# Performance work log

Hardware: AMD Instinct MI355X
Metric: run time of the kernel (lower is better)

The kernel has to match this reference:

```python
import jax, jax.numpy as jnp
from jax import lax
import numpy as np

B = 2048
N = 10  # wires on q_device0
C64 = jnp.complex64

# fixed gate matrices (qubit ordering matches wire-list order)
S_ = jnp.array([[1, 0], [0, 1j]], C64)
T_ = jnp.array([[1, 0], [0, np.exp(1j * np.pi / 4)]], C64)
SX_ = 0.5 * jnp.array([[1 + 1j, 1 - 1j], [1 - 1j, 1 + 1j]], C64)
Y_ = jnp.array([[0, -1j], [1j, 0]], C64)
CNOT_ = jnp.array([[1, 0, 0, 0], [0, 1, 0, 0], [0, 0, 0, 1], [0, 0, 1, 0]], C64)
CZ_ = jnp.diag(jnp.array([1, 1, 1, -1], C64))
CY_ = jnp.array([[1, 0, 0, 0], [0, 1, 0, 0], [0, 0, 0, -1j], [0, 0, 1j, 0]], C64)
SWAP_ = jnp.array([[1, 0, 0, 0], [0, 0, 1, 0], [0, 1, 0, 0], [0, 0, 0, 1]], C64)
_cs = np.eye(8); _cs[[5, 6]] = _cs[[6, 5]]  # CSWAP: |101> <-> |110>
CSWAP_ = jnp.array(_cs, C64)
_tf = np.eye(8); _tf[[6, 7]] = _tf[[7, 6]]  # Toffoli: |110> <-> |111>
TOFF_ = jnp.array(_tf, C64)

# parametrized single-qubit gate builders; t scalar -> [2,2], t [B] -> [B,2,2]
def _rx(t):
    c = jnp.cos(t / 2).astype(C64)
    s = -1j * jnp.sin(t / 2).astype(C64)
    return jnp.stack([jnp.stack([c, s], -1), jnp.stack([s, c], -1)], -2)

def _ry(t):
    c = jnp.cos(t / 2).astype(C64)
    s = jnp.sin(t / 2).astype(C64)
    return jnp.stack([jnp.stack([c, -s], -1), jnp.stack([s, c], -1)], -2)

def _rz(t):
    a = jnp.exp(-0.5j * t.astype(C64))
    b = jnp.exp(0.5j * t.astype(C64))
    z = jnp.zeros_like(a)
    return jnp.stack([jnp.stack([a, z], -1), jnp.stack([z, b], -1)], -2)

def _phase(t):
    e = jnp.exp(1j * t.astype(C64))
    o = jnp.ones_like(e)
    z = jnp.zeros_like(e)
    return jnp.stack([jnp.stack([o, z], -1), jnp.stack([z, e], -1)], -2)

def _rot(phi, th, om):  # RZ(om) RY(th) RZ(phi), pennylane/torchquantum convention
    c = jnp.cos(th / 2).astype(C64)
    s = jnp.sin(th / 2).astype(C64)
    p = phi.astype(C64); w = om.astype(C64)
    m00 = jnp.exp(-0.5j * (p + w)) * c
    m01 = -jnp.exp(0.5j * (p - w)) * s
    m10 = jnp.exp(-0.5j * (p - w)) * s
    m11 = jnp.exp(0.5j * (p + w)) * c
    return jnp.stack([jnp.stack([m00, m01], -1), jnp.stack([m10, m11], -1)], -2)

def _apply1(psi, U, w):  # psi: [B]+(2,)*N, U: [2,2] or [B,2,2]
    s = jnp.moveaxis(psi, w + 1, 1)
    if U.ndim == 2:
        s = jnp.einsum('ij,bj...->bi...', U, s)
    else:
        s = jnp.einsum('bij,bj...->bi...', U, s)
    return jnp.moveaxis(s, 1, w + 1)

def _applyk(psi, U, wires):  # fixed k-qubit gate, U: [2^k, 2^k]
    k = len(wires)
    axes = tuple(w + 1 for w in wires)
    s = jnp.moveaxis(psi, axes, tuple(range(1, k + 1)))
    sh = s.shape
    s = s.reshape((sh[0], 2 ** k) + sh[k + 1:])
    s = jnp.einsum('ij,bj...->bi...', U, s)
    return jnp.moveaxis(s.reshape(sh), tuple(range(1, k + 1)), axes)

def _forward(x, conv1_w, conv1_b, conv2_w, conv2_b, fc1_w, fc1_b, fc2_w, fc2_b,
             theta0, theta_rz, theta_ps, rot_p):
    dn = ('NCHW', 'OIHW', 'NCHW')
    h = lax.conv_general_dilated(x, conv1_w, (1, 1), 'VALID', dimension_numbers=dn)
    h = jax.nn.relu(h + conv1_b[None, :, None, None])
    h = lax.conv_general_dilated(h, conv2_w, (1, 1), 'VALID', dimension_numbers=dn)
    h = jax.nn.relu(h + conv2_b[None, :, None, None])
    h = lax.reduce_window(h, -jnp.inf, lax.max, (1, 1, 2, 2), (1, 1, 2, 2), 'VALID')
    h = h.reshape(h.shape[0], -1)  # [B, 9216], dropout = identity (eval)
    h = jax.nn.relu(h @ fc1_w.T + fc1_b)
    a = jax.nn.sigmoid(h @ fc2_w.T + fc2_b) * (2.0 * np.pi)  # angles [B, 10]
    bsz = a.shape[0]
    psi = jnp.zeros((bsz, 2 ** N), C64).at[:, 0].set(1.0).reshape((bsz,) + (2,) * N)
    trz = jnp.reshape(theta_rz, ())
    tps = jnp.reshape(theta_ps, ())
    for k in range(N):                      # TrainableRxAll
        psi = _apply1(psi, _rx(theta0[k]), k)
    for k in range(N):                      # RxAll with input angles
        psi = _apply1(psi, _rx(a[:, k]), k)
    psi = _apply1(psi, _rx(a[:, 1]), 1)
    psi = _apply1(psi, _rx(jnp.asarray(-np.pi / 4, jnp.float32)), 5)  # q_layer2 fixed
    psi = _apply1(psi, _ry(a[:, 2]), 2)
    psi = _apply1(psi, _rz(a[:, 3]), 3)
    psi = _apply1(psi, S_, 4)
    psi = _apply1(psi, T_, 5)
    psi = _apply1(psi, _rz(trz), 6)         # q_layer3
    psi = _apply1(psi, SX_, 7)
    # (q_device1 ops on a separate 3-wire device do not affect the output)
    psi = _applyk(psi, CZ_, (0, 5))
    psi = _applyk(psi, CNOT_, (0, 5))
    psi = _applyk(psi, CY_, (0, 5))
    psi = _applyk(psi, CY_, (3, 8))         # q_layer4
    psi = _applyk(psi, SWAP_, (2, 3))
    psi = _applyk(psi, CSWAP_, (4, 5, 6))
    psi = _applyk(psi, TOFF_, (8, 5, 0))    # q_layer5
    psi = _apply1(psi, _phase(tps), 8)      # q_layer6
    psi = _apply1(psi, _phase(a[:, 7]), 7)
    psi = _apply1(psi, _rot(rot_p[0], rot_p[1], rot_p[2]), 4)  # q_layer7
    psi = _apply1(psi, _rot(a[:, 6], a[:, 7], a[:, 8]), 5)
    axes = tuple(range(1, N + 1))
    evs = [jnp.real(jnp.sum(jnp.conj(psi) * _apply1(psi, Y_, k), axis=axes))
           for k in range(N)]
    ev = jnp.stack(evs, -1)                 # [B, 10] <Y_k>
    return jax.nn.log_softmax(ev, axis=1)


def setup_inputs() -> dict:
    key = jax.random.key(0)
    ks = jax.random.split(key, 13)
    return {
        'x': jax.random.normal(ks[0], (B, 1, 28, 28), jnp.float32),
        'conv1_w': jax.random.normal(ks[1], (32, 1, 3, 3), jnp.float32) * 0.2,
        'conv1_b': jnp.zeros((32,), jnp.float32),
        'conv2_w': jax.random.normal(ks[2], (64, 32, 3, 3), jnp.float32) * 0.05,
        'conv2_b': jnp.zeros((64,), jnp.float32),
        'fc1_w': jax.random.normal(ks[3], (128, 9216), jnp.float32) * 0.01,
        'fc1_b': jnp.zeros((128,), jnp.float32),
        'fc2_w': jax.random.normal(ks[4], (10, 128), jnp.float32) * 0.1,
        'fc2_b': jnp.zeros((10,), jnp.float32),
        'theta0': jax.random.normal(ks[5], (10,), jnp.float32),
        'theta_rz': jax.random.normal(ks[6], (1,), jnp.float32),
        'theta_ps': jax.random.normal(ks[7], (1,), jnp.float32),
        'rot_p': jax.random.normal(ks[8], (3,), jnp.float32),
    }


def reference(x, conv1_w, conv1_b, conv2_w, conv2_b, fc1_w, fc1_b, fc2_w, fc2_b,
              theta0, theta_rz, theta_ps, rot_p):
    return _forward(x, conv1_w, conv1_b, conv2_w, conv2_b, fc1_w, fc1_b, fc2_w, fc2_b,
                    theta0, theta_rz, theta_ps, rot_p)
```

## Files before the change

### kernel.cpp

```cpp
#include <hip/hip_runtime.h>
#include <math.h>

typedef short short8 __attribute__((ext_vector_type(8)));
typedef float f32x4 __attribute__((ext_vector_type(4)));
typedef float f32x16 __attribute__((ext_vector_type(16)));

#define GLB_CP(p) ((const __attribute__((address_space(1))) void*)(p))
#define LDS_CP(p) ((__attribute__((address_space(3))) void*)(p))

__device__ __forceinline__ float2 cmul(float2 a, float2 b) {
    return make_float2(a.x * b.x - a.y * b.y, a.x * b.y + a.y * b.x);
}

__device__ __forceinline__ ushort f2bf(float f) {
    uint u = __float_as_uint(f);
    uint r = (u + 0x7FFFu + ((u >> 16) & 1u)) >> 16;
    return (ushort)r;
}

__global__ __launch_bounds__(256) void prep_kernel(
    const float* __restrict__ c2w, const float* __restrict__ f1w,
    ushort* __restrict__ wt2, ushort* __restrict__ wf1)
{
    int i = blockIdx.x * 256 + threadIdx.x;
    if (i < 18432) {
        int icl = i & 7;
        int t = i >> 3;
        int oc = t & 63;
        int t2 = t >> 6;
        int icg = t2 & 3;
        int tap = t2 >> 2;
        int ic = icg * 8 + icl;
        wt2[i] = f2bf(c2w[(oc * 32 + ic) * 9 + tap]);
    } else if (i < 18432 + 1179648) {
        int j = i - 18432;
        wf1[j] = f2bf(f1w[j]);
    }
}

__global__ __launch_bounds__(256) void conv1_kernel(
    const float* __restrict__ x, const float* __restrict__ w1,
    const float* __restrict__ b1, ushort* __restrict__ h1b)
{
    __shared__ float wl[288];
    __shared__ float bl[32];
    int tid = threadIdx.x;
    for (int e = tid; e < 288; e += 256) wl[e] = w1[e];
    if (tid < 32) bl[tid] = b1[tid];
    __syncthreads();
    int e = blockIdx.x * 256 + tid;
    int icg = e & 3;
    int t = e >> 2;
    int pix = t % 676;
    int b = t / 676;
    int y = pix / 26, xc = pix % 26;
    const float* xp = x + b * 784 + y * 28 + xc;
    float in9[9];
#pragma unroll
    for (int ky = 0; ky < 3; ++ky)
#pragma unroll
        for (int kx = 0; kx < 3; ++kx) in9[ky * 3 + kx] = xp[ky * 28 + kx];
    short8 outv;
#pragma unroll
    for (int o = 0; o < 8; ++o) {
        int oc = icg * 8 + o;
        float acc = bl[oc];
#pragma unroll
        for (int k = 0; k < 9; ++k) acc = fmaf(in9[k], wl[oc * 9 + k], acc);
        outv[o] = (short)f2bf(fmaxf(acc, 0.f));
    }
    *(short8*)&h1b[((b * 4 + icg) * 676 + pix) * 8] = outv;
}

#define EPILOG(ACC0, ACC1, RX, RY)                                                         \
    {                                                                                      \
        int pcolb = (RX) * 4 + 2 * hi;                                                     \
        _Pragma("unroll")                                                                  \
        for (int q = 0; q < 2; ++q) {                                                      \
            int prow = (RY) * 2 + q;                                                       \
            int bs = 8 * q;                                                                \
            float m00 = fmaxf(fmaxf(ACC0[bs], ACC0[bs + 1]), fmaxf(ACC0[bs + 4], ACC0[bs + 5])); \
            float m01 = fmaxf(fmaxf(ACC0[bs + 2], ACC0[bs + 3]), fmaxf(ACC0[bs + 6], ACC0[bs + 7])); \
            uint pk0 = (uint)f2bf(fmaxf(m00 + bias0, 0.f)) | ((uint)f2bf(fmaxf(m01 + bias0, 0.f)) << 16); \
            *(uint*)&pout[lo * 144 + prow * 12 + pcolb] = pk0;                             \
            float m10 = fmaxf(fmaxf(ACC1[bs], ACC1[bs + 1]), fmaxf(ACC1[bs + 4], ACC1[bs + 5])); \
            float m11 = fmaxf(fmaxf(ACC1[bs + 2], ACC1[bs + 3]), fmaxf(ACC1[bs + 6], ACC1[bs + 7])); \
            uint pk1 = (uint)f2bf(fmaxf(m10 + bias1, 0.f)) | ((uint)f2bf(fmaxf(m11 + bias1, 0.f)) << 16); \
            *(uint*)&pout[(lo + 32) * 144 + prow * 12 + pcolb] = pk1;                      \
        }                                                                                  \
    }

__global__ __launch_bounds__(384, 2) void conv2_persist(
    const ushort* __restrict__ h1b, const ushort* __restrict__ wt2,
    const float* __restrict__ c2b, ushort* __restrict__ pooled)
{
    __shared__ __attribute__((aligned(16))) ushort wt_lds[18432];
    __shared__ __attribute__((aligned(16))) ushort in_lds[2][22016];
    int cu = blockIdx.x;
    int tid = threadIdx.x;
    int wave = tid >> 6;
    int lane = tid & 63;
    int lo = lane & 31;
    int hi = lane >> 5;

    for (int c = wave; c < 36; c += 6) {
        const ushort* src = wt2 + (size_t)(c * 64 + lane) * 8;
        __builtin_amdgcn_global_load_lds(GLB_CP(src), LDS_CP(wt_lds + c * 512), 16, 0, 0);
    }
    {
        const ushort* base = h1b + (size_t)(cu * 8) * 21632;
        for (int c = wave; c < 43; c += 6) {
            int e = c * 64 + lane;
            if (e > 2703) e = 2703;
            __builtin_amdgcn_global_load_lds(GLB_CP(base + (size_t)e * 8),
                                             LDS_CP(in_lds[0] + c * 512), 16, 0, 0);
        }
    }
    float bias0 = c2b[lo];
    float bias1 = c2b[lo + 32];
    __syncthreads();

    short8 A0r[9][2];
#pragma unroll
    for (int tap = 0; tap < 9; ++tap)
#pragma unroll
        for (int ks = 0; ks < 2; ++ks)
            A0r[tap][ks] = *(const short8*)&wt_lds[((tap * 4 + ks * 2 + hi) * 64 + lo) * 8];

    int pb[3];
#pragma unroll
    for (int i = 0; i < 3; ++i) {
        int r = wave + 6 * i;
        int rx = r % 3, ry = r / 3;
        int xcoord = rx * 8 + (lo & 7);
        int ycoord = ry * 4 + (lo >> 3);
        pb[i] = ycoord * 26 + xcoord;
    }
    int rx0 = wave % 3, ry0 = wave / 3;
    int rx1 = (wave + 6) % 3, ry1 = (wave + 6) / 3;
    int rx2 = (wave + 12) % 3, ry2 = (wave + 12) / 3;

    for (int j = 0; j < 8; ++j) {
        if (j < 7) {
            const ushort* base = h1b + (size_t)(cu * 8 + j + 1) * 21632;
            ushort* dst = in_lds[(j + 1) & 1];
            for (int c = wave; c < 43; c += 6) {
                int e = c * 64 + lane;
                if (e > 2703) e = 2703;
                __builtin_amdgcn_global_load_lds(GLB_CP(base + (size_t)e * 8),
                                                 LDS_CP(dst + c * 512), 16, 0, 0);
            }
        }

        const ushort* ib = in_lds[j & 1];
        f32x16 aA0 = (f32x16)0.f, aA1 = (f32x16)0.f;
        f32x16 aB0 = (f32x16)0.f, aB1 = (f32x16)0.f;
        f32x16 aC0 = (f32x16)0.f, aC1 = (f32x16)0.f;

#pragma unroll
        for (int tap = 0; tap < 9; ++tap) {
            int off = (tap / 3) * 26 + (tap % 3);
#pragma unroll
            for (int ks = 0; ks < 2; ++ks) {
                short8 a0 = A0r[tap][ks];
                short8 a1 = *(const short8*)&wt_lds[((tap * 4 + ks * 2 + hi) * 64 + 32 + lo) * 8];
                const ushort* ip = &ib[((ks * 2 + hi) * 676 + off) * 8];
                short8 b0 = *(const short8*)(ip + pb[0] * 8);
                short8 b1 = *(const short8*)(ip + pb[1] * 8);
                short8 b2 = *(const short8*)(ip + pb[2] * 8);
                aA0 = __builtin_amdgcn_mfma_f32_32x32x16_bf16(b0, a0, aA0, 0, 0, 0);
                aA1 = __builtin_amdgcn_mfma_f32_32x32x16_bf16(b0, a1, aA1, 0, 0, 0);
                aB0 = __builtin_amdgcn_mfma_f32_32x32x16_bf16(b1, a0, aB0, 0, 0, 0);
                aB1 = __builtin_amdgcn_mfma_f32_32x32x16_bf16(b1, a1, aB1, 0, 0, 0);
                aC0 = __builtin_amdgcn_mfma_f32_32x32x16_bf16(b2, a0, aC0, 0, 0, 0);
                aC1 = __builtin_amdgcn_mfma_f32_32x32x16_bf16(b2, a1, aC1, 0, 0, 0);
            }
        }

        ushort* pout = pooled + (size_t)(cu * 8 + j) * 9216;
        EPILOG(aA0, aA1, rx0, ry0)
        EPILOG(aB0, aB1, rx1, ry1)
        EPILOG(aC0, aC1, rx2, ry2)
        __syncthreads();
    }
}

__global__ __launch_bounds__(256) void fc1_mfma(
    const ushort* __restrict__ pooled, const ushort* __restrict__ wf1,
    float* __restrict__ part)
{
    int bx = blockIdx.x, by = blockIdx.y;
    int tid = threadIdx.x;
    int wid = tid >> 6, lane = tid & 63;
    int lo = lane & 15, hi = lane >> 4;
    int m0 = bx * 32;
    int kb = by * 2304;

    f32x4 acc[2][2];
#pragma unroll
    for (int mt = 0; mt < 2; ++mt)
#pragma unroll
        for (int j = 0; j < 2; ++j) acc[mt][j] = (f32x4)0.f;

    const ushort* arow0 = pooled + (size_t)(m0 + lo) * 9216 + kb + hi * 8;
    const ushort* arow1 = arow0 + 16 * 9216;
    const ushort* brow0 = wf1 + (size_t)(wid * 32 + lo) * 9216 + kb + hi * 8;
    const ushort* brow1 = brow0 + 16 * 9216;

    for (int kt = 0; kt < 72; ++kt) {
        short8 a0 = *(const short8*)(arow0 + kt * 32);
        short8 a1 = *(const short8*)(arow1 + kt * 32);
        short8 b0 = *(const short8*)(brow0 + kt * 32);
        short8 b1 = *(const short8*)(brow1 + kt * 32);
        acc[0][0] = __builtin_amdgcn_mfma_f32_16x16x32_bf16(a0, b0, acc[0][0], 0, 0, 0);
        acc[1][0] = __builtin_amdgcn_mfma_f32_16x16x32_bf16(a1, b0, acc[1][0], 0, 0, 0);
        acc[0][1] = __builtin_amdgcn_mfma_f32_16x16x32_bf16(a0, b1, acc[0][1], 0, 0, 0);
        acc[1][1] = __builtin_amdgcn_mfma_f32_16x16x32_bf16(a1, b1, acc[1][1], 0, 0, 0);
    }
    float* pp = part + (size_t)by * 262144;
#pragma unroll
    for (int mt = 0; mt < 2; ++mt)
#pragma unroll
        for (int j = 0; j < 2; ++j)
#pragma unroll
            for (int r = 0; r < 4; ++r)
                pp[(m0 + mt * 16 + hi * 4 + r) * 128 + wid * 32 + j * 16 + lo] = acc[mt][j][r];
}

__global__ __launch_bounds__(256) void fc1_reduce_kernel(
    const float* __restrict__ part, const float* __restrict__ bias,
    float* __restrict__ outp)
{
    int idx = blockIdx.x * 256 + threadIdx.x;
    float s = 0.f;
#pragma unroll
    for (int ks = 0; ks < 4; ++ks) s += part[ks * 262144 + idx];
    outp[idx] = fmaxf(s + bias[idx & 127], 0.f);
}

__global__ __launch_bounds__(256) void fc2_kernel(
    const float* __restrict__ h, const float* __restrict__ w,
    const float* __restrict__ bias, float* __restrict__ ang)
{
    int idx = blockIdx.x * 256 + threadIdx.x;
    if (idx >= 20480) return;
    int b = idx / 10, n = idx % 10;
    const float* hp = h + b * 128;
    const float* wp = w + n * 128;
    float s = bias[n];
    for (int k = 0; k < 128; ++k) s = fmaf(hp[k], wp[k], s);
    ang[idx] = 6.28318530718f / (1.f + expf(-s));
}

__device__ __forceinline__ void apply_rot2(float2* s, int p, float2 m00, float2 m01,
                                           float2 m10, float2 m11, int tid)
{
    for (int q = tid; q < 512; q += 256) {
        int i0 = ((q >> p) << (p + 1)) | (q & ((1 << p) - 1));
        int i1 = i0 | (1 << p);
        float2 aa = s[i0], bb = s[i1];
        s[i0] = make_float2(m00.x * aa.x - m00.y * aa.y + m01.x * bb.x - m01.y * bb.y,
                            m00.x * aa.y + m00.y * aa.x + m01.x * bb.y + m01.y * bb.x);
        s[i1] = make_float2(m10.x * aa.x - m10.y * aa.y + m11.x * bb.x - m11.y * bb.y,
                            m10.x * aa.y + m10.y * aa.x + m11.x * bb.y + m11.y * bb.x);
    }
}

__global__ __launch_bounds__(256) void quantum_kernel(
    const float* __restrict__ ang, const float* __restrict__ theta0,
    const float* __restrict__ theta_rz, const float* __restrict__ theta_ps,
    const float* __restrict__ rot_p, float* __restrict__ out)
{
    __shared__ float2 s[1024];
    __shared__ float red[40];
    __shared__ float P[64];
    int b = blockIdx.x;
    int tid = threadIdx.x;

    if (tid < 13) {
        if (tid < 10) {
            int k = tid;
            float ak = ang[b * 10 + k];
            float th = theta0[k] + ak;
            if (k == 1) th += ak;
            if (k == 5) th -= 0.78539816339745f;
            float c, sn; sincosf(0.5f * th, &sn, &c);
            float2 v0 = make_float2(c, 0.f), v1 = make_float2(0.f, -sn);
            if (k == 0) v1 = make_float2(-sn, 0.f);
            if (k == 2) { float ca, sa; sincosf(0.5f * ak, &sa, &ca);
                float2 n0 = make_float2(ca * v0.x - sa * v1.x, ca * v0.y - sa * v1.y);
                float2 n1 = make_float2(sa * v0.x + ca * v1.x, sa * v0.y + ca * v1.y);
                v0 = n0; v1 = n1; }
            if (k == 3) { float ca, sa; sincosf(0.5f * ak, &sa, &ca);
                v0 = cmul(v0, make_float2(ca, -sa));
                v1 = cmul(v1, make_float2(ca, sa)); }
            if (k == 4) { float2 t = v1; v1 = make_float2(-t.y, t.x); }
            if (k == 5) { const float r = 0.70710678118655f;
                float2 t = v1; v1 = make_float2(r * (t.x - t.y), r * (t.x + t.y)); }
            if (k == 6) { float ca, sa; sincosf(0.5f * theta_rz[0], &sa, &ca);
                v0 = cmul(v0, make_float2(ca, -sa));
                v1 = cmul(v1, make_float2(ca, sa)); }
            if (k == 7) { float2 p = v0, q = v1;
                v0 = make_float2(0.5f * ((p.x - p.y) + (q.x + q.y)),
                                 0.5f * ((p.x + p.y) + (q.y - q.x)));
                v1 = make_float2(0.5f * ((p.x + p.y) + (q.x - q.y)),
                                 0.5f * ((p.y - p.x) + (q.x + q.y)));
                float c2, s2; sincosf(ak, &s2, &c2);
                v1 = cmul(v1, make_float2(c2, s2)); }
            P[k * 4 + 0] = v0.x; P[k * 4 + 1] = v0.y;
            P[k * 4 + 2] = v1.x; P[k * 4 + 3] = v1.y;
        } else if (tid == 10) {
            float c1, s1; sincosf(theta_ps[0], &s1, &c1);
            P[40] = c1; P[41] = s1;
        } else if (tid == 11) {
            float c, sn; sincosf(0.5f * rot_p[1], &sn, &c);
            float A = 0.5f * (rot_p[0] + rot_p[2]), Bv = 0.5f * (rot_p[0] - rot_p[2]);
            float cA, sA; sincosf(A, &sA, &cA);
            float cB, sB; sincosf(Bv, &sB, &cB);
            P[44] = cA * c;  P[45] = -sA * c;
            P[46] = -cB * sn; P[47] = -sB * sn;
            P[48] = cB * sn;  P[49] = -sB * sn;
            P[50] = cA * c;  P[51] = sA * c;
        } else {
            float a6 = ang[b * 10 + 6], a7 = ang[b * 10 + 7], a8 = ang[b * 10 + 8];
            float c, sn; sincosf(0.5f * a7, &sn, &c);
            float A = 0.5f * (a6 + a8), Bv = 0.5f * (a6 - a8);
            float cA, sA; sincosf(A, &sA, &cA);
            float cB, sB; sincosf(Bv, &sB, &cB);
            P[52] = cA * c;  P[53] = -sA * c;
            P[54] = -cB * sn; P[55] = -sB * sn;
            P[56] = cB * sn;  P[57] = -sB * sn;
            P[58] = cA * c;  P[59] = sA * c;
        }
    }
    __syncthreads();

    float2 v[10][2];
#pragma unroll
    for (int k = 0; k < 10; ++k) {
        int slot = (k == 2) ? 3 : (k == 3) ? 2 : k;
        v[k][0] = make_float2(P[slot * 4], P[slot * 4 + 1]);
        v[k][1] = make_float2(P[slot * 4 + 2], P[slot * 4 + 3]);
    }

    for (int i = tid; i < 1024; i += 256) {
        float2 c = ((i >> 9) & 1) ? v[0][1] : v[0][0];
#pragma unroll
        for (int k = 1; k < 10; ++k) {
            float2 vk = ((i >> (9 - k)) & 1) ? v[k][1] : v[k][0];
            c = cmul(c, vk);
        }
        s[i] = c;
    }
    __syncthreads();

    {
        int j = tid;
        float2 p1 = make_float2(P[40], P[41]);
        int i0 = (j & 1) | (((j >> 1) & 31) << 2) | (((j >> 6) & 3) << 8) | 128;
        int i1 = i0 | 2;
        float2 t0 = s[i0], t1 = s[i1];
        s[i0] = make_float2(t1.y, -t1.x);
        s[i1] = cmul(make_float2(-t0.y, t0.x), p1);
        int i2 = (j & 1) | 2 | (((j >> 1) & 31) << 2) | (((j >> 6) & 3) << 8);
        s[i2] = cmul(s[i2], p1);
    }
    __syncthreads();
    if (tid < 128) {
        int j = tid;
        int i0 = (j & 7) | 16 | 32 | (((j >> 3) & 15) << 6);
        int i1 = i0 ^ 0x18;
        float2 t0 = s[i0], t1 = s[i1];
        s[i0] = t1; s[i1] = t0;
    }
    __syncthreads();
    if (tid < 128) {
        int j = tid;
        int i0 = (j & 1) | 2 | (((j >> 1) & 3) << 2) | 16 | (((j >> 3) & 15) << 5);
        int i1 = i0 | 512;
        float2 t0 = s[i0], t1 = s[i1];
        s[i0] = t1; s[i1] = t0;
    }
    __syncthreads();
    apply_rot2(s, 5, make_float2(P[44], P[45]), make_float2(P[46], P[47]),
               make_float2(P[48], P[49]), make_float2(P[50], P[51]), tid);
    __syncthreads();
    apply_rot2(s, 4, make_float2(P[52], P[53]), make_float2(P[54], P[55]),
               make_float2(P[56], P[57]), make_float2(P[58], P[59]), tid);
    __syncthreads();

    int wave = tid >> 6;
    for (int k = 0; k < 10; ++k) {
        int p = 9 - k;
        float part = 0.f;
        for (int q = tid; q < 512; q += 256) {
            int i0 = ((q >> p) << (p + 1)) | (q & ((1 << p) - 1));
            int i1 = i0 | (1 << p);
            float2 aa = s[i0], bb = s[i1];
            part += aa.x * bb.y - aa.y * bb.x;
        }
        part *= 2.f;
#pragma unroll
        for (int off = 32; off > 0; off >>= 1)
            part += __shfl_down(part, off, 64);
        if ((tid & 63) == 0) red[k * 4 + wave] = part;
    }
    __syncthreads();
    if (tid == 0) {
        float ev[10];
        float mx = -1e30f;
#pragma unroll
        for (int k = 0; k < 10; ++k) {
            ev[k] = red[k * 4] + red[k * 4 + 1] + red[k * 4 + 2] + red[k * 4 + 3];
            mx = fmaxf(mx, ev[k]);
        }
        float sum = 0.f;
#pragma unroll
        for (int k = 0; k < 10; ++k) sum += expf(ev[k] - mx);
        float lse = mx + logf(sum);
#pragma unroll
        for (int k = 0; k < 10; ++k) out[b * 10 + k] = ev[k] - lse;
    }
}

extern "C" void kernel_launch(void* const* d_in, const int* in_sizes, int n_in,
                              void* d_out, int out_size, void* d_ws, size_t ws_size,
                              hipStream_t stream)
{
    (void)in_sizes; (void)n_in; (void)out_size; (void)ws_size;
    const float* x    = (const float*)d_in[0];
    const float* c1w  = (const float*)d_in[1];
    const float* c1b  = (const float*)d_in[2];
    const float* c2w  = (const float*)d_in[3];
    const float* c2b  = (const float*)d_in[4];
    const float* f1w  = (const float*)d_in[5];
    const float* f1b  = (const float*)d_in[6];
    const float* f2w  = (const float*)d_in[7];
    const float* f2b  = (const float*)d_in[8];
    const float* th0  = (const float*)d_in[9];
    const float* trz  = (const float*)d_in[10];
    const float* tps  = (const float*)d_in[11];
    const float* rotp = (const float*)d_in[12];
    float* out = (float*)d_out;

    char* ws = (char*)d_ws;
    ushort* h1b    = (ushort*)(ws);
    ushort* pooled = (ushort*)(ws + 88604672);
    ushort* wt2    = (ushort*)(ws + 126353408);
    ushort* wf1    = (ushort*)(ws + 126390272);
    float*  part   = (float*)(ws + 128749568);
    float*  fc1o   = (float*)(ws + 132943872);
    float*  ang    = (float*)(ws + 133992448);

    prep_kernel<<<4680, 256, 0, stream>>>(c2w, f1w, wt2, wf1);
    conv1_kernel<<<21632, 256, 0, stream>>>(x, c1w, c1b, h1b);
    conv2_persist<<<256, 384, 0, stream>>>(h1b, wt2, c2b, pooled);
    fc1_mfma<<<dim3(64, 4), 256, 0, stream>>>(pooled, wf1, part);
    fc1_reduce_kernel<<<1024, 256, 0, stream>>>(part, f1b, fc1o);
    fc2_kernel<<<80, 256, 0, stream>>>(fc1o, f2w, f2b, ang);
    quantum_kernel<<<2048, 256, 0, stream>>>(ang, th0, trz, tps, rotp, out);
}
```

Before: 151.3 us.

## Fuse prep into conv1 and fold fc1 reduce and fc2 into quantum kernel

The weight-conversion prep kernel is merged into the conv1 launch as extra blocks. The fc1 split-K reduction, bias, ReLU and the fc2 layer with its sigmoid are moved into the per-sample quantum kernel, which now computes its ten angles in shared memory. This cuts the launch count from seven to four and drops the fc1o and ang round trips through global memory. The cost is that fc2 runs on only 10 threads per block serially over 128 inputs, which lengthens the front of each quantum block.

```diff
diff --git a/kernel.cpp b/kernel.cpp
--- a/kernel.cpp
+++ b/kernel.cpp
@@ -18,37 +18,37 @@
     return (ushort)r;
 }
 
-__global__ __launch_bounds__(256) void prep_kernel(
+__global__ __launch_bounds__(256) void conv1_prep_kernel(
+    const float* __restrict__ x, const float* __restrict__ w1,
+    const float* __restrict__ b1, ushort* __restrict__ h1b,
     const float* __restrict__ c2w, const float* __restrict__ f1w,
     ushort* __restrict__ wt2, ushort* __restrict__ wf1)
 {
-    int i = blockIdx.x * 256 + threadIdx.x;
-    if (i < 18432) {
-        int icl = i & 7;
-        int t = i >> 3;
-        int oc = t & 63;
-        int t2 = t >> 6;
-        int icg = t2 & 3;
-        int tap = t2 >> 2;
-        int ic = icg * 8 + icl;
-        wt2[i] = f2bf(c2w[(oc * 32 + ic) * 9 + tap]);
-    } else if (i < 18432 + 1179648) {
-        int j = i - 18432;
-        wf1[j] = f2bf(f1w[j]);
-    }
-}
-
-__global__ __launch_bounds__(256) void conv1_kernel(
-    const float* __restrict__ x, const float* __restrict__ w1,
-    const float* __restrict__ b1, ushort* __restrict__ h1b)
-{
     __shared__ float wl[288];
     __shared__ float bl[32];
+    int blk = blockIdx.x;
     int tid = threadIdx.x;
+    if (blk >= 21632) {
+        int i = (blk - 21632) * 256 + tid;
+        if (i < 18432) {
+            int icl = i & 7;
+            int t = i >> 3;
+            int oc = t & 63;
+            int t2 = t >> 6;
+            int icg = t2 & 3;
+            int tap = t2 >> 2;
+            int ic = icg * 8 + icl;
+            wt2[i] = f2bf(c2w[(oc * 32 + ic) * 9 + tap]);
+        } else if (i < 18432 + 1179648) {
+            int j = i - 18432;
+            wf1[j] = f2bf(f1w[j]);
+        }
+        return;
+    }
     for (int e = tid; e < 288; e += 256) wl[e] = w1[e];
     if (tid < 32) bl[tid] = b1[tid];
     __syncthreads();
-    int e = blockIdx.x * 256 + tid;
+    int e = blk * 256 + tid;
     int icg = e & 3;
     int t = e >> 2;
     int pix = t % 676;
@@ -227,31 +227,6 @@
                 pp[(m0 + mt * 16 + hi * 4 + r) * 128 + wid * 32 + j * 16 + lo] = acc[mt][j][r];
 }
 
-__global__ __launch_bounds__(256) void fc1_reduce_kernel(
-    const float* __restrict__ part, const float* __restrict__ bias,
-    float* __restrict__ outp)
-{
-    int idx = blockIdx.x * 256 + threadIdx.x;
-    float s = 0.f;
-#pragma unroll
-    for (int ks = 0; ks < 4; ++ks) s += part[ks * 262144 + idx];
-    outp[idx] = fmaxf(s + bias[idx & 127], 0.f);
-}
-
-__global__ __launch_bounds__(256) void fc2_kernel(
-    const float* __restrict__ h, const float* __restrict__ w,
-    const float* __restrict__ bias, float* __restrict__ ang)
-{
-    int idx = blockIdx.x * 256 + threadIdx.x;
-    if (idx >= 20480) return;
-    int b = idx / 10, n = idx % 10;
-    const float* hp = h + b * 128;
-    const float* wp = w + n * 128;
-    float s = bias[n];
-    for (int k = 0; k < 128; ++k) s = fmaf(hp[k], wp[k], s);
-    ang[idx] = 6.28318530718f / (1.f + expf(-s));
-}
-
 __device__ __forceinline__ void apply_rot2(float2* s, int p, float2 m00, float2 m01,
                                            float2 m10, float2 m11, int tid)
 {
@@ -267,20 +242,38 @@
 }
 
 __global__ __launch_bounds__(256) void quantum_kernel(
-    const float* __restrict__ ang, const float* __restrict__ theta0,
-    const float* __restrict__ theta_rz, const float* __restrict__ theta_ps,
-    const float* __restrict__ rot_p, float* __restrict__ out)
+    const float* __restrict__ part, const float* __restrict__ f1b,
+    const float* __restrict__ f2w, const float* __restrict__ f2b,
+    const float* __restrict__ theta0, const float* __restrict__ theta_rz,
+    const float* __restrict__ theta_ps, const float* __restrict__ rot_p,
+    float* __restrict__ out)
 {
     __shared__ float2 s[1024];
     __shared__ float red[40];
     __shared__ float P[64];
+    __shared__ float h[128];
+    __shared__ float angs[16];
     int b = blockIdx.x;
     int tid = threadIdx.x;
+
+    if (tid < 128) {
+        float v = part[0 * 262144 + b * 128 + tid] + part[1 * 262144 + b * 128 + tid]
+                + part[2 * 262144 + b * 128 + tid] + part[3 * 262144 + b * 128 + tid];
+        h[tid] = fmaxf(v + f1b[tid], 0.f);
+    }
+    __syncthreads();
+    if (tid < 10) {
+        const float* wp = f2w + tid * 128;
+        float sacc = f2b[tid];
+        for (int k = 0; k < 128; ++k) sacc = fmaf(h[k], wp[k], sacc);
+        angs[tid] = 6.28318530718f / (1.f + expf(-sacc));
+    }
+    __syncthreads();
 
     if (tid < 13) {
         if (tid < 10) {
             int k = tid;
-            float ak = ang[b * 10 + k];
+            float ak = angs[k];
             float th = theta0[k] + ak;
             if (k == 1) th += ak;
             if (k == 5) th -= 0.78539816339745f;
@@ -322,7 +315,7 @@
             P[48] = cB * sn;  P[49] = -sB * sn;
             P[50] = cA * c;  P[51] = sA * c;
         } else {
-            float a6 = ang[b * 10 + 6], a7 = ang[b * 10 + 7], a8 = ang[b * 10 + 8];
+            float a6 = angs[6], a7 = angs[7], a8 = angs[8];
             float c, sn; sincosf(0.5f * a7, &sn, &c);
             float A = 0.5f * (a6 + a8), Bv = 0.5f * (a6 - a8);
             float cA, sA; sincosf(A, &sA, &cA);
@@ -392,18 +385,18 @@
     int wave = tid >> 6;
     for (int k = 0; k < 10; ++k) {
         int p = 9 - k;
-        float part = 0.f;
+        float part_ = 0.f;
         for (int q = tid; q < 512; q += 256) {
             int i0 = ((q >> p) << (p + 1)) | (q & ((1 << p) - 1));
             int i1 = i0 | (1 << p);
             float2 aa = s[i0], bb = s[i1];
-            part += aa.x * bb.y - aa.y * bb.x;
-        }
-        part *= 2.f;
+            part_ += aa.x * bb.y - aa.y * bb.x;
+        }
+        part_ *= 2.f;
 #pragma unroll
         for (int off = 32; off > 0; off >>= 1)
-            part += __shfl_down(part, off, 64);
-        if ((tid & 63) == 0) red[k * 4 + wave] = part;
+            part_ += __shfl_down(part_, off, 64);
+        if ((tid & 63) == 0) red[k * 4 + wave] = part_;
     }
     __syncthreads();
     if (tid == 0) {
@@ -449,14 +442,9 @@
     ushort* wt2    = (ushort*)(ws + 126353408);
     ushort* wf1    = (ushort*)(ws + 126390272);
     float*  part   = (float*)(ws + 128749568);
-    float*  fc1o   = (float*)(ws + 132943872);
-    float*  ang    = (float*)(ws + 133992448);
-
-    prep_kernel<<<4680, 256, 0, stream>>>(c2w, f1w, wt2, wf1);
-    conv1_kernel<<<21632, 256, 0, stream>>>(x, c1w, c1b, h1b);
+
+    conv1_prep_kernel<<<26312, 256, 0, stream>>>(x, c1w, c1b, h1b, c2w, f1w, wt2, wf1);
     conv2_persist<<<256, 384, 0, stream>>>(h1b, wt2, c2b, pooled);
     fc1_mfma<<<dim3(64, 4), 256, 0, stream>>>(pooled, wf1, part);
-    fc1_reduce_kernel<<<1024, 256, 0, stream>>>(part, f1b, fc1o);
-    fc2_kernel<<<80, 256, 0, stream>>>(fc1o, f2w, f2b, ang);
-    quantum_kernel<<<2048, 256, 0, stream>>>(ang, th0, trz, tps, rotp, out);
-}
+    quantum_kernel<<<2048, 256, 0, stream>>>(part, f1b, f2w, f2b, th0, trz, tps, rotp, out);
+}
```

Measured after the change: 140.5 us. 1.08x faster.
